# Kernel optimization log

Measured on AMD Instinct MI355X. Metric: run time of the kernel, lower is better.

The kernel has to match this reference:

```python
import jax, jax.numpy as jnp
import numpy as np

B, LC, I, H, O, T = 512, 512, 64, 100, 64, 256


def setup_inputs() -> dict:
    key = jax.random.key(0)
    ks = jax.random.split(key, 10)
    context = jax.random.normal(ks[0], (B, LC, I), dtype=jnp.float32)
    context_lengths = jnp.clip(jax.random.randint(ks[1], (B,), 0, LC), 1, LC)
    s_e = 1.0 / np.sqrt(I)   # embed init scale (pytorch Linear default)
    s_h = 1.0 / np.sqrt(H)
    u = lambda k, shp, s: jax.random.uniform(k, shp, jnp.float32, -s, s)
    return {
        "context": context,
        "context_lengths": context_lengths,
        "t_steps": T,
        "W_embed": u(ks[2], (H, I), s_e), "b_embed": u(ks[3], (H,), s_e),
        "W_ih": u(ks[4], (3 * H, H), s_h), "b_ih": u(ks[5], (3 * H,), s_h),
        "W_hh": u(ks[6], (3 * H, H), s_h), "b_hh": u(ks[7], (3 * H,), s_h),
        "W_proj": u(ks[8], (O, H), s_h), "b_proj": u(ks[9], (O,), s_h),
    }


def _gru_cell(h, x_pre, W_hh, b_hh):
    # x_pre: precomputed x @ W_ih.T + b_ih, shape [B, 3H]
    gh = h @ W_hh.T + b_hh
    ri, zi, ni = jnp.split(x_pre, 3, axis=-1)
    rh, zh, nh = jnp.split(gh, 3, axis=-1)
    r = jax.nn.sigmoid(ri + rh)
    z = jax.nn.sigmoid(zi + zh)
    n = jnp.tanh(ni + r * nh)
    return (1.0 - z) * n + z * h


def reference(context, context_lengths, t_steps, W_embed, b_embed,
              W_ih, W_hh, b_ih, b_hh, W_proj, b_proj):
    Bc = context.shape[0]
    # ---- encode ----
    x = context @ W_embed.T + b_embed                      # [B, Lc, H]
    x_pre = x @ W_ih.T + b_ih                              # [B, Lc, 3H] (input gates precomputed)

    def enc_step(h, xp):
        h = _gru_cell(h, xp, W_hh, b_hh)
        return h, h

    h_init = jnp.zeros((Bc, W_hh.shape[1]), context.dtype)
    _, hs = jax.lax.scan(enc_step, h_init, jnp.swapaxes(x_pre, 0, 1))  # hs: [Lc, B, H]
    h0 = hs[context_lengths - 1, jnp.arange(Bc)]           # last valid hidden per example

    z0 = h0 @ W_proj.T + b_proj                            # [B, O]

    def dec_step(carry, _):
        h, z = carry
        xp = (z @ W_embed.T + b_embed) @ W_ih.T + b_ih
        h = _gru_cell(h, xp, W_hh, b_hh)
        z = h @ W_proj.T + b_proj
        return (h, z), z

    _, zs = jax.lax.scan(dec_step, (h0, z0), None, length=t_steps)  # [T, B, O]
    out = jnp.concatenate([z0[None], zs], axis=0)          # [T+1, B, O]
    return jnp.swapaxes(out, 0, 1)                         # [B, T+1, O]
```

## Files before the change

### kernel.cpp

```cpp
#include <hip/hip_runtime.h>


#define B_  512
#define LC_ 512
#define I_  64
#define H_  100
#define O_  64
#define T_  256
#define H3  300

#define WS_WC   0
#define WS_BC   19200
#define WS_WD   19500
#define WS_BD   49500
#define WS_PERM 49800

typedef float v2f __attribute__((ext_vector_type(2)));

__global__ __launch_bounds__(64) void prep1(const float* __restrict__ Wih,
                                            const float* __restrict__ bih,
                                            const float* __restrict__ Wemb,
                                            const float* __restrict__ bemb,
                                            float* __restrict__ ws) {
    int j = blockIdx.x;
    int i = threadIdx.x;
    float acc = 0.f;
    for (int k = 0; k < H_; ++k) acc += Wih[j * H_ + k] * Wemb[k * I_ + i];
    ws[WS_WC + j * I_ + i] = acc;
    if (i == 0) {
        float b = bih[j];
        for (int k = 0; k < H_; ++k) b += Wih[j * H_ + k] * bemb[k];
        ws[WS_BC + j] = b;
    }
}

__global__ __launch_bounds__(128) void prep2(const float* __restrict__ Wproj,
                                             const float* __restrict__ bproj,
                                             float* __restrict__ ws) {
    int j = blockIdx.x;
    int u = threadIdx.x;
    const float* Wc = ws + WS_WC;
    if (u < H_) {
        float acc = 0.f;
        for (int o = 0; o < O_; ++o) acc += Wc[j * I_ + o] * Wproj[o * H_ + u];
        ws[WS_WD + j * H_ + u] = acc;
    }
    if (u == 0) {
        float b = ws[WS_BC + j];
        for (int o = 0; o < O_; ++o) b += Wc[j * I_ + o] * bproj[o];
        ws[WS_BD + j] = b;
    }
}

__global__ __launch_bounds__(512) void sortk(const int* __restrict__ lens,
                                             int* __restrict__ perm) {
    __shared__ int sl[B_];
    int tid = threadIdx.x;
    sl[tid] = lens[tid];
    __syncthreads();
    int li = sl[tid];
    int rank = 0;
    for (int j = 0; j < B_; ++j) {
        int lj = sl[j];
        rank += (lj > li) || (lj == li && j < tid);
    }
    perm[rank] = tid;
}

__device__ __forceinline__ float sigm_(float x) { return 1.f / (1.f + __expf(-x)); }
__device__ __forceinline__ float tanh_(float x) {
    float t = __expf(-2.f * fabsf(x));
    float r = (1.f - t) / (1.f + t);
    return (x >= 0.f) ? r : -r;
}

template <int CTRL>
__device__ __forceinline__ float dppmov_(float x) {
    return __int_as_float(
        __builtin_amdgcn_mov_dpp(__float_as_int(x), CTRL, 0xF, 0xF, true));
}

template <int N>
__device__ __forceinline__ float dotred_(const v2f* __restrict__ w, const v2f* __restrict__ v) {
    v2f a = {0.f, 0.f};
    #pragma unroll
    for (int j = 0; j < N; ++j) a = w[j] * v[j] + a;
    float s = a.x + a.y;
    s += dppmov_<0xB1>(s);
    return s;
}

__global__ __attribute__((amdgpu_flat_work_group_size(512, 512)))
__attribute__((amdgpu_waves_per_eu(2, 2)))
void rnn7(const float* __restrict__ ctx, const int* __restrict__ lens,
          const float* __restrict__ Whh, const float* __restrict__ bhh,
          const float* __restrict__ Wproj, const float* __restrict__ bproj,
          const float* __restrict__ ws, float* __restrict__ out) {

    const int tid = threadIdx.x;
    const int l   = tid & 1;
    const int g   = tid >> 1;
    const bool wl = (l == 0);

    const int* perm = (const int*)(ws + WS_PERM);
    const int e0 = perm[blockIdx.x];
    const int e1 = perm[511 - blockIdx.x];
    const int len0 = lens[e0], len1 = lens[e1];

    __shared__ __align__(16) float sh[2][104];
    __shared__ __align__(16) float sctx[2][64];
    __shared__ float sdot[2][672];
    __shared__ float sbh[H3], sbx[H3];

    const int r0 = g;
    const int r1 = 256 + g;
    const int r2 = 512 + g;
    const bool p1hh = (g < 44);
    const bool p2e  = (g < 88);
    const bool p2d  = (g < 152);

    v2f wA[25], wB[25], wC[25];
    {
        const float* rowA = Whh + r0 * H_ + 50 * l;
        #pragma unroll
        for (int j = 0; j < 25; ++j) wA[j] = *(const v2f*)(rowA + 2 * j);
        if (p1hh) {
            const float* rowB = Whh + r1 * H_ + 50 * l;
            #pragma unroll
            for (int j = 0; j < 25; ++j) wB[j] = *(const v2f*)(rowB + 2 * j);
        } else {
            const float* rowB = ws + WS_WC + (r1 - H3) * I_ + 32 * l;
            #pragma unroll
            for (int j = 0; j < 16; ++j) wB[j] = *(const v2f*)(rowB + 2 * j);
        }
        if (p2e) {
            const float* rowC = ws + WS_WC + (r2 - H3) * I_ + 32 * l;
            #pragma unroll
            for (int j = 0; j < 16; ++j) wC[j] = *(const v2f*)(rowC + 2 * j);
        }
    }

    const int ge = (tid >= 100);
    const int gi = tid - (ge ? 100 : 0);
    const int hs = (gi < 50) ? gi : gi + 2;
    const int lenG = ge ? len1 : len0;
    float hreg = 0.f;

    const int oe = (tid >> 6) & 1;
    const int oo = tid & 63;
    float* oute = out + (size_t)(oe ? e1 : e0) * (T_ + 1) * O_;
    float bpr = 0.f;
    if (tid >= 256 && tid < 384) bpr = bproj[oo];

    const int pe = (tid >> 4) & 1;
    const int pi = tid & 15;
    const float4* pctx = (const float4*)(ctx + (size_t)(pe ? e1 : e0) * LC_ * I_);
    const int lenP = pe ? len1 : len0;

    if (tid < 208) ((float*)sh)[tid] = 0.f;
    if (tid < H3) { sbh[tid] = bhh[tid]; sbx[tid] = (ws + WS_BC)[tid]; }
    if (tid >= 384 && tid < 416) *(float4*)&sctx[pe][4 * pi] = pctx[pi];
    __syncthreads();

    for (int t = 0; t < len0; ++t) {
        float4 pf;
        const bool hp = (tid >= 384 && tid < 416) && (t + 1 < lenP);
        if (hp) pf = pctx[(t + 1) * 16 + pi];

        #pragma unroll
        for (int e = 0; e < 2; ++e) {
            if (e == 0 || t < len1) {
                v2f hv[25], cv[16];
                #pragma unroll
                for (int q = 0; q < 12; ++q) {
                    float4 f = *(const float4*)&sh[e][52 * l + 4 * q];
                    hv[2 * q]     = v2f{f.x, f.y};
                    hv[2 * q + 1] = v2f{f.z, f.w};
                }
                hv[24] = *(const v2f*)&sh[e][52 * l + 48];
                #pragma unroll
                for (int q = 0; q < 8; ++q) {
                    float4 f = *(const float4*)&sctx[e][32 * l + 4 * q];
                    cv[2 * q]     = v2f{f.x, f.y};
                    cv[2 * q + 1] = v2f{f.z, f.w};
                }

                float a0 = dotred_<25>(wA, hv);
                if (wl) sdot[e][r0] = a0;
                float a1 = p1hh ? dotred_<25>(wB, hv) : dotred_<16>(wB, cv);
                if (wl) sdot[e][r1] = a1;
                if (p2e) {
                    float a2 = dotred_<16>(wC, cv);
                    if (wl) sdot[e][r2] = a2;
                }
            }
        }
        __syncthreads();
        if (tid < 200 && t < lenG) {
            const float* sd = sdot[ge];
            float gr = sd[gi]       + sbh[gi];
            float gz = sd[gi + 100] + sbh[gi + 100];
            float gn = sd[gi + 200] + sbh[gi + 200];
            float xr = sd[gi + 300] + sbx[gi];
            float xz = sd[gi + 400] + sbx[gi + 100];
            float xn = sd[gi + 500] + sbx[gi + 200];
            float r = sigm_(xr + gr);
            float z = sigm_(xz + gz);
            float n = tanh_(xn + r * gn);
            hreg = (1.f - z) * n + z * hreg;
            sh[ge][hs] = hreg;
        }
        if (hp) *(float4*)&sctx[pe][4 * pi] = pf;
        __syncthreads();
    }

    {
        if (!p1hh) {
            const float* rowB = ws + WS_WD + (r1 - H3) * H_ + 50 * l;
            #pragma unroll
            for (int j = 0; j < 25; ++j) wB[j] = *(const v2f*)(rowB + 2 * j);
        }
        if (g < 88) {
            const float* rowC = ws + WS_WD + (r2 - H3) * H_ + 50 * l;
            #pragma unroll
            for (int j = 0; j < 25; ++j) wC[j] = *(const v2f*)(rowC + 2 * j);
        } else if (g < 152) {
            const float* rowC = Wproj + (g - 88) * H_ + 50 * l;
            #pragma unroll
            for (int j = 0; j < 25; ++j) wC[j] = *(const v2f*)(rowC + 2 * j);
        }
    }
    if (tid < H3) sbx[tid] = (ws + WS_BD)[tid];

    for (int t = 0; t <= T_; ++t) {
        #pragma unroll
        for (int e = 0; e < 2; ++e) {
            v2f hv[25];
            #pragma unroll
            for (int q = 0; q < 12; ++q) {
                float4 f = *(const float4*)&sh[e][52 * l + 4 * q];
                hv[2 * q]     = v2f{f.x, f.y};
                hv[2 * q + 1] = v2f{f.z, f.w};
            }
            hv[24] = *(const v2f*)&sh[e][52 * l + 48];

            float a0 = dotred_<25>(wA, hv);
            if (wl) sdot[e][r0] = a0;
            float a1 = dotred_<25>(wB, hv);
            if (wl) sdot[e][r1] = a1;
            if (p2d) {
                float a2 = dotred_<25>(wC, hv);
                if (wl) sdot[e][r2] = a2;
            }
        }
        __syncthreads();
        if (tid >= 256 && tid < 384) {
            oute[t * O_ + oo] = sdot[oe][600 + oo] + bpr;
        }
        if (t == T_) break;
        if (tid < 200) {
            const float* sd = sdot[ge];
            float gr = sd[gi]       + sbh[gi];
            float gz = sd[gi + 100] + sbh[gi + 100];
            float gn = sd[gi + 200] + sbh[gi + 200];
            float xr = sd[gi + 300] + sbx[gi];
            float xz = sd[gi + 400] + sbx[gi + 100];
            float xn = sd[gi + 500] + sbx[gi + 200];
            float r = sigm_(xr + gr);
            float z = sigm_(xz + gz);
            float n = tanh_(xn + r * gn);
            hreg = (1.f - z) * n + z * hreg;
            sh[ge][hs] = hreg;
        }
        __syncthreads();
    }
}

extern "C" void kernel_launch(void* const* d_in, const int* in_sizes, int n_in,
                              void* d_out, int out_size, void* d_ws, size_t ws_size,
                              hipStream_t stream) {
    (void)in_sizes; (void)n_in; (void)out_size; (void)ws_size;
    const float* ctx  = (const float*)d_in[0];
    const int*   lens = (const int*)d_in[1];
    const float* Wemb = (const float*)d_in[3];
    const float* bemb = (const float*)d_in[4];
    const float* Wih  = (const float*)d_in[5];
    const float* bih  = (const float*)d_in[6];
    const float* Whh  = (const float*)d_in[7];
    const float* bhh  = (const float*)d_in[8];
    const float* Wpr  = (const float*)d_in[9];
    const float* bpr  = (const float*)d_in[10];
    float* ws  = (float*)d_ws;
    float* out = (float*)d_out;

    prep1<<<H3, 64, 0, stream>>>(Wih, bih, Wemb, bemb, ws);
    prep2<<<H3, 128, 0, stream>>>(Wpr, bpr, ws);
    sortk<<<1, 512, 0, stream>>>(lens, (int*)(ws + WS_PERM));
    rnn7<<<256, 512, 0, stream>>>(ctx, lens, Whh, bhh, Wpr, bpr, ws, out);
}
```

Before: 900.1 us.

## Split each dot-product row across four lanes instead of two

Changes the work split so that four lanes cooperate on each weight-row dot product, each handling a quarter of the hidden or context vector, with a two-step DPP reduction. Each thread now owns up to six row-quarters rather than three row-halves, which shortens the serial FMA chain per row. The hidden-state shared layout is re-padded to 28-float segments to match. In exchange it adds an extra DPP reduction step per row, requires more per-thread register indexing, and reads more shared-memory broadcasts per lane.

```diff
diff --git a/kernel.cpp b/kernel.cpp
--- a/kernel.cpp
+++ b/kernel.cpp
@@ -79,27 +79,37 @@
     return __int_as_float(
         __builtin_amdgcn_mov_dpp(__float_as_int(x), CTRL, 0xF, 0xF, true));
 }
-
-template <int N>
-__device__ __forceinline__ float dotred_(const v2f* __restrict__ w, const v2f* __restrict__ v) {
+__device__ __forceinline__ float red4_(float a) {
+    a += dppmov_<0xB1>(a);
+    a += dppmov_<0x4E>(a);
+    return a;
+}
+
+__device__ __forceinline__ float dotH_(const v2f* __restrict__ w2, float w1,
+                                       const v2f* __restrict__ hv2, float h24) {
     v2f a = {0.f, 0.f};
     #pragma unroll
-    for (int j = 0; j < N; ++j) a = w[j] * v[j] + a;
-    float s = a.x + a.y;
-    s += dppmov_<0xB1>(s);
-    return s;
+    for (int j = 0; j < 12; ++j) a = w2[j] * hv2[j] + a;
+    return red4_(fmaf(w1, h24, a.x + a.y));
+}
+__device__ __forceinline__ float dotC_(const v2f* __restrict__ w2,
+                                       const v2f* __restrict__ cv2) {
+    v2f a = {0.f, 0.f};
+    #pragma unroll
+    for (int j = 0; j < 8; ++j) a = w2[j] * cv2[j] + a;
+    return red4_(a.x + a.y);
 }
 
 __global__ __attribute__((amdgpu_flat_work_group_size(512, 512)))
 __attribute__((amdgpu_waves_per_eu(2, 2)))
-void rnn7(const float* __restrict__ ctx, const int* __restrict__ lens,
+void rnn8(const float* __restrict__ ctx, const int* __restrict__ lens,
           const float* __restrict__ Whh, const float* __restrict__ bhh,
           const float* __restrict__ Wproj, const float* __restrict__ bproj,
           const float* __restrict__ ws, float* __restrict__ out) {
 
     const int tid = threadIdx.x;
-    const int l   = tid & 1;
-    const int g   = tid >> 1;
+    const int l   = tid & 3;
+    const int g   = tid >> 2;
     const bool wl = (l == 0);
 
     const int* perm = (const int*)(ws + WS_PERM);
@@ -107,42 +117,49 @@
     const int e1 = perm[511 - blockIdx.x];
     const int len0 = lens[e0], len1 = lens[e1];
 
-    __shared__ __align__(16) float sh[2][104];
+    __shared__ __align__(16) float sh[2][112];
     __shared__ __align__(16) float sctx[2][64];
     __shared__ float sdot[2][672];
     __shared__ float sbh[H3], sbx[H3];
 
-    const int r0 = g;
-    const int r1 = 256 + g;
-    const int r2 = 512 + g;
-    const bool p1hh = (g < 44);
-    const bool p2e  = (g < 88);
-    const bool p2d  = (g < 152);
-
-    v2f wA[25], wB[25], wC[25];
+    const bool p2hh = (g < 44);
+    const bool p4a  = (g < 88);
+    const bool p5a  = (g < 24);
+
+    v2f   w2[6][12];
+    float w1[6];
     {
-        const float* rowA = Whh + r0 * H_ + 50 * l;
-        #pragma unroll
-        for (int j = 0; j < 25; ++j) wA[j] = *(const v2f*)(rowA + 2 * j);
-        if (p1hh) {
-            const float* rowB = Whh + r1 * H_ + 50 * l;
-            #pragma unroll
-            for (int j = 0; j < 25; ++j) wB[j] = *(const v2f*)(rowB + 2 * j);
+        const float* r0 = Whh + g * H_ + 25 * l;
+        const float* r1 = Whh + (128 + g) * H_ + 25 * l;
+        #pragma unroll
+        for (int j = 0; j < 12; ++j) {
+            w2[0][j] = v2f{r0[2 * j], r0[2 * j + 1]};
+            w2[1][j] = v2f{r1[2 * j], r1[2 * j + 1]};
+        }
+        w1[0] = r0[24]; w1[1] = r1[24];
+        if (p2hh) {
+            const float* r2 = Whh + (256 + g) * H_ + 25 * l;
+            #pragma unroll
+            for (int j = 0; j < 12; ++j) w2[2][j] = v2f{r2[2 * j], r2[2 * j + 1]};
+            w1[2] = r2[24];
         } else {
-            const float* rowB = ws + WS_WC + (r1 - H3) * I_ + 32 * l;
-            #pragma unroll
-            for (int j = 0; j < 16; ++j) wB[j] = *(const v2f*)(rowB + 2 * j);
-        }
-        if (p2e) {
-            const float* rowC = ws + WS_WC + (r2 - H3) * I_ + 32 * l;
-            #pragma unroll
-            for (int j = 0; j < 16; ++j) wC[j] = *(const v2f*)(rowC + 2 * j);
+            const float* r2 = ws + WS_WC + (g - 44) * I_ + 16 * l;
+            #pragma unroll
+            for (int j = 0; j < 8; ++j) w2[2][j] = v2f{r2[2 * j], r2[2 * j + 1]};
+        }
+        const float* r3 = ws + WS_WC + (84 + g) * I_ + 16 * l;
+        #pragma unroll
+        for (int j = 0; j < 8; ++j) w2[3][j] = v2f{r3[2 * j], r3[2 * j + 1]};
+        if (p4a) {
+            const float* r4 = ws + WS_WC + (212 + g) * I_ + 16 * l;
+            #pragma unroll
+            for (int j = 0; j < 8; ++j) w2[4][j] = v2f{r4[2 * j], r4[2 * j + 1]};
         }
     }
 
     const int ge = (tid >= 100);
     const int gi = tid - (ge ? 100 : 0);
-    const int hs = (gi < 50) ? gi : gi + 2;
+    const int hs = 28 * (gi / 25) + (gi % 25);
     const int lenG = ge ? len1 : len0;
     float hreg = 0.f;
 
@@ -157,7 +174,7 @@
     const float4* pctx = (const float4*)(ctx + (size_t)(pe ? e1 : e0) * LC_ * I_);
     const int lenP = pe ? len1 : len0;
 
-    if (tid < 208) ((float*)sh)[tid] = 0.f;
+    if (tid < 224) ((float*)sh)[tid] = 0.f;
     if (tid < H3) { sbh[tid] = bhh[tid]; sbx[tid] = (ws + WS_BC)[tid]; }
     if (tid >= 384 && tid < 416) *(float4*)&sctx[pe][4 * pi] = pctx[pi];
     __syncthreads();
@@ -170,28 +187,35 @@
         #pragma unroll
         for (int e = 0; e < 2; ++e) {
             if (e == 0 || t < len1) {
-                v2f hv[25], cv[16];
+                v2f hv2[12], cv2[8];
+                float h24;
                 #pragma unroll
-                for (int q = 0; q < 12; ++q) {
-                    float4 f = *(const float4*)&sh[e][52 * l + 4 * q];
-                    hv[2 * q]     = v2f{f.x, f.y};
-                    hv[2 * q + 1] = v2f{f.z, f.w};
+                for (int q = 0; q < 6; ++q) {
+                    float4 f = *(const float4*)&sh[e][28 * l + 4 * q];
+                    hv2[2 * q]     = v2f{f.x, f.y};
+                    hv2[2 * q + 1] = v2f{f.z, f.w};
                 }
-                hv[24] = *(const v2f*)&sh[e][52 * l + 48];
+                h24 = sh[e][28 * l + 24];
                 #pragma unroll
-                for (int q = 0; q < 8; ++q) {
-                    float4 f = *(const float4*)&sctx[e][32 * l + 4 * q];
-                    cv[2 * q]     = v2f{f.x, f.y};
-                    cv[2 * q + 1] = v2f{f.z, f.w};
+                for (int q = 0; q < 4; ++q) {
+                    float4 f = *(const float4*)&sctx[e][16 * l + 4 * q];
+                    cv2[2 * q]     = v2f{f.x, f.y};
+                    cv2[2 * q + 1] = v2f{f.z, f.w};
                 }
 
-                float a0 = dotred_<25>(wA, hv);
-                if (wl) sdot[e][r0] = a0;
-                float a1 = p1hh ? dotred_<25>(wB, hv) : dotred_<16>(wB, cv);
-                if (wl) sdot[e][r1] = a1;
-                if (p2e) {
-                    float a2 = dotred_<16>(wC, cv);
-                    if (wl) sdot[e][r2] = a2;
+                float a0 = dotH_(w2[0], w1[0], hv2, h24);
+                float a1 = dotH_(w2[1], w1[1], hv2, h24);
+                float a2 = p2hh ? dotH_(w2[2], w1[2], hv2, h24) : dotC_(w2[2], cv2);
+                float a3 = dotC_(w2[3], cv2);
+                if (wl) {
+                    sdot[e][g] = a0;
+                    sdot[e][128 + g] = a1;
+                    sdot[e][256 + g] = a2;
+                    sdot[e][384 + g] = a3;
+                }
+                if (p4a) {
+                    float a4 = dotC_(w2[4], cv2);
+                    if (wl) sdot[e][512 + g] = a4;
                 }
             }
         }
@@ -215,19 +239,26 @@
     }
 
     {
-        if (!p1hh) {
-            const float* rowB = ws + WS_WD + (r1 - H3) * H_ + 50 * l;
-            #pragma unroll
-            for (int j = 0; j < 25; ++j) wB[j] = *(const v2f*)(rowB + 2 * j);
-        }
-        if (g < 88) {
-            const float* rowC = ws + WS_WD + (r2 - H3) * H_ + 50 * l;
-            #pragma unroll
-            for (int j = 0; j < 25; ++j) wC[j] = *(const v2f*)(rowC + 2 * j);
-        } else if (g < 152) {
-            const float* rowC = Wproj + (g - 88) * H_ + 50 * l;
-            #pragma unroll
-            for (int j = 0; j < 25; ++j) wC[j] = *(const v2f*)(rowC + 2 * j);
+        if (!p2hh) {
+            const float* r2 = ws + WS_WD + (g - 44) * H_ + 25 * l;
+            #pragma unroll
+            for (int j = 0; j < 12; ++j) w2[2][j] = v2f{r2[2 * j], r2[2 * j + 1]};
+            w1[2] = r2[24];
+        }
+        const float* r3 = ws + WS_WD + (84 + g) * H_ + 25 * l;
+        #pragma unroll
+        for (int j = 0; j < 12; ++j) w2[3][j] = v2f{r3[2 * j], r3[2 * j + 1]};
+        w1[3] = r3[24];
+        const float* r4 = p4a ? (ws + WS_WD + (212 + g) * H_ + 25 * l)
+                              : (Wproj + (g - 88) * H_ + 25 * l);
+        #pragma unroll
+        for (int j = 0; j < 12; ++j) w2[4][j] = v2f{r4[2 * j], r4[2 * j + 1]};
+        w1[4] = r4[24];
+        if (p5a) {
+            const float* r5 = Wproj + (40 + g) * H_ + 25 * l;
+            #pragma unroll
+            for (int j = 0; j < 12; ++j) w2[5][j] = v2f{r5[2 * j], r5[2 * j + 1]};
+            w1[5] = r5[24];
         }
     }
     if (tid < H3) sbx[tid] = (ws + WS_BD)[tid];
@@ -235,22 +266,31 @@
     for (int t = 0; t <= T_; ++t) {
         #pragma unroll
         for (int e = 0; e < 2; ++e) {
-            v2f hv[25];
-            #pragma unroll
-            for (int q = 0; q < 12; ++q) {
-                float4 f = *(const float4*)&sh[e][52 * l + 4 * q];
-                hv[2 * q]     = v2f{f.x, f.y};
-                hv[2 * q + 1] = v2f{f.z, f.w};
+            v2f hv2[12];
+            float h24;
+            #pragma unroll
+            for (int q = 0; q < 6; ++q) {
+                float4 f = *(const float4*)&sh[e][28 * l + 4 * q];
+                hv2[2 * q]     = v2f{f.x, f.y};
+                hv2[2 * q + 1] = v2f{f.z, f.w};
             }
-            hv[24] = *(const v2f*)&sh[e][52 * l + 48];
-
-            float a0 = dotred_<25>(wA, hv);
-            if (wl) sdot[e][r0] = a0;
-            float a1 = dotred_<25>(wB, hv);
-            if (wl) sdot[e][r1] = a1;
-            if (p2d) {
-                float a2 = dotred_<25>(wC, hv);
-                if (wl) sdot[e][r2] = a2;
+            h24 = sh[e][28 * l + 24];
+
+            float a0 = dotH_(w2[0], w1[0], hv2, h24);
+            float a1 = dotH_(w2[1], w1[1], hv2, h24);
+            float a2 = dotH_(w2[2], w1[2], hv2, h24);
+            float a3 = dotH_(w2[3], w1[3], hv2, h24);
+            float a4 = dotH_(w2[4], w1[4], hv2, h24);
+            if (wl) {
+                sdot[e][g] = a0;
+                sdot[e][128 + g] = a1;
+                sdot[e][256 + g] = a2;
+                sdot[e][384 + g] = a3;
+                sdot[e][512 + g] = a4;
+            }
+            if (p5a) {
+                float a5 = dotH_(w2[5], w1[5], hv2, h24);
+                if (wl) sdot[e][640 + g] = a5;
             }
         }
         __syncthreads();
@@ -296,5 +336,5 @@
     prep1<<<H3, 64, 0, stream>>>(Wih, bih, Wemb, bemb, ws);
     prep2<<<H3, 128, 0, stream>>>(Wpr, bpr, ws);
     sortk<<<1, 512, 0, stream>>>(lens, (int*)(ws + WS_PERM));
-    rnn7<<<256, 512, 0, stream>>>(ctx, lens, Whh, bhh, Wpr, bpr, ws, out);
-}
+    rnn8<<<256, 512, 0, stream>>>(ctx, lens, Whh, bhh, Wpr, bpr, ws, out);
+}
```

Measured after the change: 831.2 us. 7.6% less time.
